# Optimization experiments

Measured on AMD Instinct MI355X. Metric: run time of the kernel, lower is better.

The kernel has to match this reference:

```python
import jax, jax.numpy as jnp
import numpy as np

B, S, T, D, H, DF, E = 16, 1024, 512, 512, 8, 2048, 4
DH = D // H
EPS = 1e-5


def setup_inputs() -> dict:
    key = jax.random.key(0)
    ks = iter(jax.random.split(key, 64))

    def nrm(shape, scale=0.02):
        return jax.random.normal(next(ks), shape, dtype=jnp.float32) * scale

    inp = {
        "x": jax.random.normal(next(ks), (B, S, D), dtype=jnp.float32),
        "cross": jax.random.normal(next(ks), (B, T, D), dtype=jnp.float32),
    }
    for p in ("sa", "ca"):
        for w in ("wq", "wk", "wv", "wo"):
            inp[f"{p}_{w}"] = nrm((D, D))
            inp[f"{p}_b{w[1]}"] = jnp.zeros((D,), jnp.float32)
    inp["gate_w"] = nrm((D, E))
    inp["gate_b"] = jnp.zeros((E,), jnp.float32)
    inp["exp_w1"] = nrm((E, D, DF))
    inp["exp_b1"] = jnp.zeros((E, DF), jnp.float32)
    inp["exp_w2"] = nrm((E, DF, D))
    inp["exp_b2"] = jnp.zeros((E, D), jnp.float32)
    for i in (1, 2, 3):
        inp[f"n{i}_g"] = jnp.ones((D,), jnp.float32)
        inp[f"n{i}_b"] = jnp.zeros((D,), jnp.float32)
    return inp


def layer_norm(x, g, b):
    m = x.mean(-1, keepdims=True)
    v = x.var(-1, keepdims=True)
    return (x - m) * jax.lax.rsqrt(v + EPS) * g + b


def mha(q_in, kv_in, wq, bq, wk, bk, wv, bv, wo, bo, causal):
    Bq, Sq, _ = q_in.shape
    Sk = kv_in.shape[1]
    q = (q_in @ wq + bq).reshape(Bq, Sq, H, DH)
    k = (kv_in @ wk + bk).reshape(Bq, Sk, H, DH)
    v = (kv_in @ wv + bv).reshape(Bq, Sk, H, DH)
    scores = jnp.einsum('bshd,bthd->bhst', q, k) / jnp.sqrt(jnp.float32(DH))
    if causal:
        mask = jnp.tril(jnp.ones((Sq, Sk), dtype=bool))
        scores = jnp.where(mask, scores, jnp.float32(-1e9))
    attn = jax.nn.softmax(scores, axis=-1)
    out = jnp.einsum('bhst,bthd->bshd', attn, v).reshape(Bq, Sq, D)
    return out @ wo + bo


def moe_ffn(x, gw, gb, w1, b1, w2, b2):
    gates = jax.nn.softmax(x @ gw + gb, axis=-1)            # [B,S,E]
    h = jax.nn.relu(jnp.einsum('bsd,edf->bsef', x, w1) + b1)  # [B,S,E,DF]
    yo = jnp.einsum('bsef,efd->bsed', h, w2) + b2            # [B,S,E,D]
    y = jnp.einsum('bse,bsed->bsd', gates, yo)
    imp = gates.mean((0, 1))                                 # importance per expert
    aux = jnp.float32(E) * jnp.sum(imp * imp)                # load-balance penalty
    return y, aux


def reference(x, cross,
              sa_wq, sa_bq, sa_wk, sa_bk, sa_wv, sa_bv, sa_wo, sa_bo,
              ca_wq, ca_bq, ca_wk, ca_bk, ca_wv, ca_bv, ca_wo, ca_bo,
              gate_w, gate_b, exp_w1, exp_b1, exp_w2, exp_b2,
              n1_g, n1_b, n2_g, n2_b, n3_g, n3_b):
    # dropout is identity in eval mode
    x = x + mha(x, x, sa_wq, sa_bq, sa_wk, sa_bk, sa_wv, sa_bv, sa_wo, sa_bo, causal=True)
    x = layer_norm(x, n1_g, n1_b)
    x = x + mha(x, cross, ca_wq, ca_bq, ca_wk, ca_bk, ca_wv, ca_bv, ca_wo, ca_bo, causal=False)
    x = layer_norm(x, n2_g, n2_b)
    y, aux_loss = moe_ffn(x, gate_w, gate_b, exp_w1, exp_b1, exp_w2, exp_b2)
    out = layer_norm(x + y, n3_g, n3_b)
    return out, aux_loss
```

## Files before the change

kernel.cpp:

```cpp
#include <hip/hip_runtime.h>
#include <stdint.h>
#include <stddef.h>

typedef unsigned short bf16u;
typedef __attribute__((ext_vector_type(8))) short short8;
typedef __attribute__((ext_vector_type(4))) float f32x4;

__device__ __forceinline__ bf16u f2bf(float f) {
  union { float f; unsigned u; } v; v.f = f;
  unsigned r = v.u + 0x7FFFu + ((v.u >> 16) & 1u);
  return (bf16u)(r >> 16);
}

#define GL16(g, l) __builtin_amdgcn_global_load_lds( \
    (const __attribute__((address_space(1))) unsigned int*)(g), \
    (__attribute__((address_space(3))) unsigned int*)(l), 16, 0, 0)

enum { EPI_BF16 = 0, EPI_RELU_GATE = 1, EPI_QKV = 2, EPI_RES = 3, EPI_F32ACC = 4, EPI_KV = 5 };

template<int EPI>
__global__ __launch_bounds__(256, 3) void gemm_k(
    const bf16u* __restrict__ A, int LDA,
    const bf16u* __restrict__ BT, int LDB,
    const float* __restrict__ bias, const float* __restrict__ res,
    const float* __restrict__ gates,
    bf16u* __restrict__ o1, bf16u* __restrict__ o2, bf16u* __restrict__ o3,
    float* __restrict__ of,
    int N, int K, int slog, int egate0, int firste)
{
  __shared__ bf16u Ab[2][128 * 32];
  __shared__ bf16u Bb[2][128 * 32];
  const int tid = threadIdx.x, lane = tid & 63, w = tid >> 6;
  const int wm = w >> 1, wn = w & 1;
  const int cpx = gridDim.x >> 3;
  const int bid = (blockIdx.x & 7) * cpx + (blockIdx.x >> 3);
  const int nbt = N >> 7;
  const int mt = bid / nbt, nt = bid - mt * nbt;
  const int bm = mt << 7, bn = nt << 7;

  const int srow = lane >> 2;
  const int scol = (lane & 3) << 3;
  const bf16u* ap0 = A + (size_t)(bm + w * 16 + srow) * LDA + scol;
  const bf16u* ap1 = ap0 + (size_t)64 * LDA;
  const bf16u* bp0 = BT + (size_t)(bn + w * 16 + srow) * LDB + scol;
  const bf16u* bp1 = bp0 + (size_t)64 * LDB;

  f32x4 acc[4][4] = {};
  const int NT = K >> 5;

  GL16(ap0, &Ab[0][w * 512]);
  GL16(ap1, &Ab[0][(4 + w) * 512]);
  GL16(bp0, &Bb[0][w * 512]);
  GL16(bp1, &Bb[0][(4 + w) * 512]);
  __syncthreads();

  const int rl = lane & 15, kg = (lane >> 4) << 3;
  int cur = 0;
  for (int kt = 0; kt < NT; ++kt) {
    if (kt + 1 < NT) {
      const int ko = (kt + 1) << 5;
      const int nb = cur ^ 1;
      GL16(ap0 + ko, &Ab[nb][w * 512]);
      GL16(ap1 + ko, &Ab[nb][(4 + w) * 512]);
      GL16(bp0 + ko, &Bb[nb][w * 512]);
      GL16(bp1 + ko, &Bb[nb][(4 + w) * 512]);
    }
    short8 af[4], bfv[4];
    #pragma unroll
    for (int i = 0; i < 4; ++i)
      af[i] = *(const short8*)&Ab[cur][(wm * 64 + i * 16 + rl) * 32 + kg];
    #pragma unroll
    for (int j = 0; j < 4; ++j)
      bfv[j] = *(const short8*)&Bb[cur][(wn * 64 + j * 16 + rl) * 32 + kg];
    #pragma unroll
    for (int i = 0; i < 4; ++i)
      #pragma unroll
      for (int j = 0; j < 4; ++j)
        acc[i][j] = __builtin_amdgcn_mfma_f32_16x16x32_bf16(af[i], bfv[j], acc[i][j], 0, 0, 0);
    __syncthreads();
    cur ^= 1;
  }

  const int r0 = bm + wm * 64, c0 = bn + wn * 64;
  const int rsub = (lane >> 4) << 2;
  #pragma unroll
  for (int j = 0; j < 4; ++j) {
    const int col = c0 + j * 16 + rl;
    const float bs = bias ? bias[col] : 0.f;
    #pragma unroll
    for (int i = 0; i < 4; ++i) {
      const f32x4 v = acc[i][j];
      #pragma unroll
      for (int jj = 0; jj < 4; ++jj) {
        const int row = r0 + i * 16 + rsub + jj;
        const float val = v[jj] + bs;
        if (EPI == EPI_BF16) {
          o1[(size_t)row * N + col] = f2bf(val);
        } else if (EPI == EPI_RELU_GATE) {
          const float g = gates[(size_t)row * 4 + egate0 + (col >> 11)];
          o1[(size_t)row * N + col] = f2bf(g * (val > 0.f ? val : 0.f));
        } else if (EPI == EPI_QKV) {
          if (col < 512) o1[(size_t)row * 512 + col] = f2bf(val);
          else if (col < 1024) o2[(size_t)row * 512 + col - 512] = f2bf(val);
          else {
            const int c = col - 1024;
            const int b_ = row >> slog, t_ = row & ((1 << slog) - 1);
            o3[(((size_t)(b_ * 8 + (c >> 6)) << 6) + (size_t)(c & 63)) * ((size_t)1 << slog) + t_] = f2bf(val);
          }
        } else if (EPI == EPI_KV) {
          if (col < 512) o2[(size_t)row * 512 + col] = f2bf(val);
          else {
            const int c = col - 512;
            const int b_ = row >> slog, t_ = row & ((1 << slog) - 1);
            o3[(((size_t)(b_ * 8 + (c >> 6)) << 6) + (size_t)(c & 63)) * ((size_t)1 << slog) + t_] = f2bf(val);
          }
        } else if (EPI == EPI_RES) {
          of[(size_t)row * N + col] = res[(size_t)row * N + col] + val;
        } else {
          const size_t oi = (size_t)row * N + col;
          of[oi] = firste ? val : (of[oi] + val);
        }
      }
    }
  }
}

template<bool CAUSAL>
__global__ __launch_bounds__(256, 4) void attn_k(
    const bf16u* __restrict__ Q, const bf16u* __restrict__ Kg,
    const bf16u* __restrict__ VT, bf16u* __restrict__ O,
    int Sq, int Sk)
{
  __shared__ bf16u Kl[2][64 * 64];
  __shared__ bf16u Vl[2][64 * 64];
  __shared__ bf16u Pl[64 * 64];
  const int nqt = Sq >> 6;
  const int cpx = gridDim.x >> 3;
  const int bid = (blockIdx.x & 7) * cpx + (blockIdx.x >> 3);
  const int bh = bid / nqt;
  int qt = bid - bh * nqt;
  if (CAUSAL) qt = nqt - 1 - qt;
  const int b = bh >> 3, h = bh & 7;
  const int tid = threadIdx.x, lane = tid & 63, w = tid >> 6;
  const int rl = lane & 15, g4 = lane >> 4;

  const int qrow = qt * 64 + w * 16 + rl;
  const bf16u* qp = Q + (size_t)(b * Sq + qrow) * 512 + h * 64 + g4 * 8;
  const short8 qf0 = *(const short8*)qp;
  const short8 qf1 = *(const short8*)(qp + 32);

  f32x4 oacc[4] = {};
  float ml = -1e30f, ll = 0.f;
  const int KT = CAUSAL ? (qt + 1) : (Sk >> 6);

  const int str = tid >> 2, stc = tid & 3;
  const int sw_st = (str & 7) << 4;
  const bf16u* kq = Kg + (size_t)(b * Sk + str) * 512 + h * 64 + stc * 8;
  const bf16u* vq = VT + (size_t)(bh * 64 + str) * Sk + stc * 8;
  const int lo0 = str * 128 + ((stc * 16) ^ sw_st);
  const int lo1 = str * 128 + ((stc * 16 + 64) ^ sw_st);

  const int qr = w * 16 + rl;
  char* const pbase = (char*)Pl + qr * 128;
  const int swq = (qr & 7) << 4;

  {
    const short8 k0 = *(const short8*)kq;
    const short8 k1 = *(const short8*)(kq + 32);
    const short8 v0 = *(const short8*)vq;
    const short8 v1 = *(const short8*)(vq + 32);
    *(short8*)((char*)Kl[0] + lo0) = k0;
    *(short8*)((char*)Kl[0] + lo1) = k1;
    *(short8*)((char*)Vl[0] + lo0) = v0;
    *(short8*)((char*)Vl[0] + lo1) = v1;
  }
  __syncthreads();

  int cur = 0;
  for (int kt = 0; kt < KT; ++kt) {
    short8 nk0, nk1, nv0, nv1;
    const bool pre = (kt + 1 < KT);
    if (pre) {
      const bf16u* ks = kq + (size_t)(kt + 1) * 64 * 512;
      const bf16u* vs = vq + (kt + 1) * 64;
      nk0 = *(const short8*)ks;
      nk1 = *(const short8*)(ks + 32);
      nv0 = *(const short8*)vs;
      nv1 = *(const short8*)(vs + 32);
    }

    const bf16u* Kc = Kl[cur];
    const bf16u* Vc = Vl[cur];
    f32x4 st[4] = {};
    #pragma unroll
    for (int mi = 0; mi < 4; ++mi) {
      const int kr = mi * 16 + rl;
      const char* kb_ = (const char*)Kc + kr * 128;
      const int sw = (kr & 7) << 4;
      const short8 kf0 = *(const short8*)(kb_ + ((g4 * 16) ^ sw));
      const short8 kf1 = *(const short8*)(kb_ + ((g4 * 16 + 64) ^ sw));
      st[mi] = __builtin_amdgcn_mfma_f32_16x16x32_bf16(kf0, qf0, st[mi], 0, 0, 0);
      st[mi] = __builtin_amdgcn_mfma_f32_16x16x32_bf16(kf1, qf1, st[mi], 0, 0, 0);
    }

    const float SC = 0.125f * 1.44269504f;
    float sv[16];
    float pm = -1e30f;
    if (CAUSAL && kt == qt) {
      const int qg = qt * 64 + qr;
      #pragma unroll
      for (int mi = 0; mi < 4; ++mi)
        #pragma unroll
        for (int jj = 0; jj < 4; ++jj) {
          float s = st[mi][jj] * SC;
          const int kgi = kt * 64 + mi * 16 + g4 * 4 + jj;
          if (kgi > qg) s = -1e30f;
          sv[mi * 4 + jj] = s;
          pm = fmaxf(pm, s);
        }
    } else {
      #pragma unroll
      for (int mi = 0; mi < 4; ++mi)
        #pragma unroll
        for (int jj = 0; jj < 4; ++jj) {
          const float s = st[mi][jj] * SC;
          sv[mi * 4 + jj] = s;
          pm = fmaxf(pm, s);
        }
    }
    pm = fmaxf(pm, __shfl_xor(pm, 16));
    pm = fmaxf(pm, __shfl_xor(pm, 32));
    const float mnew = fmaxf(ml, pm);
    const float alpha = exp2f(ml - mnew);
    float ps = 0.f;
    bf16u pb[16];
    #pragma unroll
    for (int ii = 0; ii < 16; ++ii) {
      const float p = exp2f(sv[ii] - mnew);
      ps += p;
      pb[ii] = f2bf(p);
    }
    ps += __shfl_xor(ps, 16);
    ps += __shfl_xor(ps, 32);
    ll = ll * alpha + ps;
    ml = mnew;

    #pragma unroll
    for (int jj = 0; jj < 4; ++jj) {
      const float aj = __shfl(alpha, g4 * 4 + jj);
      #pragma unroll
      for (int ni = 0; ni < 4; ++ni) oacc[ni][jj] *= aj;
    }

    #pragma unroll
    for (int mi = 0; mi < 4; ++mi) {
      #pragma unroll
      for (int jp = 0; jp < 2; ++jp) {
        const unsigned pk = (unsigned)pb[mi * 4 + jp * 2] | ((unsigned)pb[mi * 4 + jp * 2 + 1] << 16);
        const int kx2 = mi * 32 + g4 * 8 + jp * 4;
        *(unsigned*)(pbase + (kx2 ^ swq)) = pk;
      }
    }
    asm volatile("s_waitcnt lgkmcnt(0)" ::: "memory");
    #pragma unroll
    for (int ks = 0; ks < 2; ++ks) {
      const short8 pf = *(const short8*)(pbase + ((g4 * 16 + ks * 64) ^ swq));
      #pragma unroll
      for (int ni = 0; ni < 4; ++ni) {
        const int vr = ni * 16 + rl;
        const short8 vf = *(const short8*)((const char*)Vc + vr * 128 + ((g4 * 16 + ks * 64) ^ ((vr & 7) << 4)));
        oacc[ni] = __builtin_amdgcn_mfma_f32_16x16x32_bf16(pf, vf, oacc[ni], 0, 0, 0);
      }
    }

    if (pre) {
      const int nb = cur ^ 1;
      *(short8*)((char*)Kl[nb] + lo0) = nk0;
      *(short8*)((char*)Kl[nb] + lo1) = nk1;
      *(short8*)((char*)Vl[nb] + lo0) = nv0;
      *(short8*)((char*)Vl[nb] + lo1) = nv1;
    }
    __syncthreads();
    cur ^= 1;
  }

  #pragma unroll
  for (int jj = 0; jj < 4; ++jj) {
    const float lj = __shfl(ll, g4 * 4 + jj);
    const float inv = 1.f / lj;
    const int row = qt * 64 + w * 16 + g4 * 4 + jj;
    #pragma unroll
    for (int ni = 0; ni < 4; ++ni)
      O[(size_t)(b * Sq + row) * 512 + h * 64 + ni * 16 + rl] = f2bf(oacc[ni][jj] * inv);
  }
}

template<bool ADD, bool BOUT>
__global__ __launch_bounds__(256, 4) void ln_k(
    const float* __restrict__ X, const float* __restrict__ Y,
    const float* __restrict__ gam, const float* __restrict__ bet,
    float* __restrict__ outf, bf16u* __restrict__ outb)
{
  const int row = blockIdx.x * 4 + (threadIdx.x >> 6);
  const int lane = threadIdx.x & 63;
  const float* xp = X + (size_t)row * 512 + lane * 8;
  float v[8];
  {
    const float4 t0 = *(const float4*)xp;
    const float4 t1 = *(const float4*)(xp + 4);
    v[0] = t0.x; v[1] = t0.y; v[2] = t0.z; v[3] = t0.w;
    v[4] = t1.x; v[5] = t1.y; v[6] = t1.z; v[7] = t1.w;
  }
  if (ADD) {
    const float* yp = Y + (size_t)row * 512 + lane * 8;
    const float4 t0 = *(const float4*)yp;
    const float4 t1 = *(const float4*)(yp + 4);
    v[0] += t0.x; v[1] += t0.y; v[2] += t0.z; v[3] += t0.w;
    v[4] += t1.x; v[5] += t1.y; v[6] += t1.z; v[7] += t1.w;
  }
  float s = 0.f, q = 0.f;
  #pragma unroll
  for (int i = 0; i < 8; ++i) { s += v[i]; q += v[i] * v[i]; }
  #pragma unroll
  for (int off = 1; off < 64; off <<= 1) {
    s += __shfl_xor(s, off);
    q += __shfl_xor(q, off);
  }
  const float mean = s * (1.f / 512.f);
  const float var = q * (1.f / 512.f) - mean * mean;
  const float rs = rsqrtf(var + 1e-5f);
  float o[8];
  #pragma unroll
  for (int i = 0; i < 8; ++i) {
    const float g = gam[lane * 8 + i], bb = bet[lane * 8 + i];
    o[i] = (v[i] - mean) * rs * g + bb;
  }
  float* op = outf + (size_t)row * 512 + lane * 8;
  *(float4*)op = make_float4(o[0], o[1], o[2], o[3]);
  *(float4*)(op + 4) = make_float4(o[4], o[5], o[6], o[7]);
  if (BOUT) {
    union { bf16u u[8]; short8 v8; } pk;
    #pragma unroll
    for (int i = 0; i < 8; ++i) pk.u[i] = f2bf(o[i]);
    *(short8*)(outb + (size_t)row * 512 + lane * 8) = pk.v8;
  }
}

__global__ __launch_bounds__(256, 4) void ln_final_k(
    const float* __restrict__ X, const float* __restrict__ Y,
    const float* __restrict__ gates, const float* __restrict__ b2,
    const float* __restrict__ gam, const float* __restrict__ bet,
    float* __restrict__ outf)
{
  const int row = blockIdx.x * 4 + (threadIdx.x >> 6);
  const int lane = threadIdx.x & 63;
  const float4 gv4 = *(const float4*)(gates + (size_t)row * 4);
  float v[8];
  {
    const float* xp = X + (size_t)row * 512 + lane * 8;
    const float* yp = Y + (size_t)row * 512 + lane * 8;
    const float4 t0 = *(const float4*)xp;
    const float4 t1 = *(const float4*)(xp + 4);
    const float4 u0 = *(const float4*)yp;
    const float4 u1 = *(const float4*)(yp + 4);
    v[0] = t0.x + u0.x; v[1] = t0.y + u0.y; v[2] = t0.z + u0.z; v[3] = t0.w + u0.w;
    v[4] = t1.x + u1.x; v[5] = t1.y + u1.y; v[6] = t1.z + u1.z; v[7] = t1.w + u1.w;
  }
  #pragma unroll
  for (int e = 0; e < 4; ++e) {
    const float ge = e == 0 ? gv4.x : e == 1 ? gv4.y : e == 2 ? gv4.z : gv4.w;
    const float4 b0 = *(const float4*)(b2 + e * 512 + lane * 8);
    const float4 b1 = *(const float4*)(b2 + e * 512 + lane * 8 + 4);
    v[0] += ge * b0.x; v[1] += ge * b0.y; v[2] += ge * b0.z; v[3] += ge * b0.w;
    v[4] += ge * b1.x; v[5] += ge * b1.y; v[6] += ge * b1.z; v[7] += ge * b1.w;
  }
  float s = 0.f, q = 0.f;
  #pragma unroll
  for (int i = 0; i < 8; ++i) { s += v[i]; q += v[i] * v[i]; }
  #pragma unroll
  for (int off = 1; off < 64; off <<= 1) {
    s += __shfl_xor(s, off);
    q += __shfl_xor(q, off);
  }
  const float mean = s * (1.f / 512.f);
  const float var = q * (1.f / 512.f) - mean * mean;
  const float rs = rsqrtf(var + 1e-5f);
  float* op = outf + (size_t)row * 512 + lane * 8;
  float o[8];
  #pragma unroll
  for (int i = 0; i < 8; ++i)
    o[i] = (v[i] - mean) * rs * gam[lane * 8 + i] + bet[lane * 8 + i];
  *(float4*)op = make_float4(o[0], o[1], o[2], o[3]);
  *(float4*)(op + 4) = make_float4(o[4], o[5], o[6], o[7]);
}

__global__ __launch_bounds__(256, 4) void gate_k(
    const float* __restrict__ X, const float* __restrict__ gw,
    const float* __restrict__ gb, float* __restrict__ gates,
    float* __restrict__ imp)
{
  __shared__ float sh[4];
  const int tid = threadIdx.x;
  if (tid < 4) sh[tid] = 0.f;
  __syncthreads();
  const int row = blockIdx.x * 4 + (tid >> 6);
  const int lane = tid & 63;
  const float* xr = X + (size_t)row * 512;
  float a0 = 0.f, a1 = 0.f, a2 = 0.f, a3 = 0.f;
  for (int d = lane; d < 512; d += 64) {
    const float xv = xr[d];
    const float4 wv = *(const float4*)(gw + d * 4);
    a0 += xv * wv.x; a1 += xv * wv.y; a2 += xv * wv.z; a3 += xv * wv.w;
  }
  #pragma unroll
  for (int off = 1; off < 64; off <<= 1) {
    a0 += __shfl_xor(a0, off); a1 += __shfl_xor(a1, off);
    a2 += __shfl_xor(a2, off); a3 += __shfl_xor(a3, off);
  }
  if (lane == 0) {
    a0 += gb[0]; a1 += gb[1]; a2 += gb[2]; a3 += gb[3];
    const float m = fmaxf(fmaxf(a0, a1), fmaxf(a2, a3));
    const float e0 = exp2f((a0 - m) * 1.44269504f);
    const float e1 = exp2f((a1 - m) * 1.44269504f);
    const float e2 = exp2f((a2 - m) * 1.44269504f);
    const float e3 = exp2f((a3 - m) * 1.44269504f);
    const float inv = 1.f / (e0 + e1 + e2 + e3);
    float* gr = gates + (size_t)row * 4;
    const float g0 = e0 * inv, g1 = e1 * inv, g2 = e2 * inv, g3 = e3 * inv;
    gr[0] = g0; gr[1] = g1; gr[2] = g2; gr[3] = g3;
    atomicAdd(&sh[0], g0); atomicAdd(&sh[1], g1);
    atomicAdd(&sh[2], g2); atomicAdd(&sh[3], g3);
  }
  __syncthreads();
  if (tid < 4) atomicAdd(&imp[tid], sh[tid]);
}

__global__ void aux_k(const float* __restrict__ imp, float* __restrict__ out) {
  if (threadIdx.x == 0 && blockIdx.x == 0) {
    float s = 0.f;
    #pragma unroll
    for (int e = 0; e < 4; ++e) { const float v = imp[e] * (1.f / 16384.f); s += v * v; }
    out[0] = 4.f * s;
  }
}

__global__ __launch_bounds__(256, 4) void conv_k(const float* __restrict__ in, bf16u* __restrict__ out) {
  const size_t i = ((size_t)blockIdx.x * 256 + threadIdx.x) * 8;
  const float4 a = *(const float4*)(in + i);
  const float4 b = *(const float4*)(in + i + 4);
  union { bf16u u[8]; short8 v; } pk;
  pk.u[0] = f2bf(a.x); pk.u[1] = f2bf(a.y); pk.u[2] = f2bf(a.z); pk.u[3] = f2bf(a.w);
  pk.u[4] = f2bf(b.x); pk.u[5] = f2bf(b.y); pk.u[6] = f2bf(b.z); pk.u[7] = f2bf(b.w);
  *(short8*)(out + i) = pk.v;
}

__global__ __launch_bounds__(256, 4) void trans_k(
    const float* __restrict__ W, bf16u* __restrict__ WT, int K, int N)
{
  __shared__ float t[32][33];
  const int tx = threadIdx.x & 31, ty = threadIdx.x >> 5;
  const int n0 = blockIdx.x * 32, k0 = blockIdx.y * 32;
  #pragma unroll
  for (int i = 0; i < 4; ++i)
    t[ty + i * 8][tx] = W[(size_t)(k0 + ty + i * 8) * N + n0 + tx];
  __syncthreads();
  #pragma unroll
  for (int i = 0; i < 4; ++i)
    WT[(size_t)(n0 + ty + i * 8) * K + k0 + tx] = f2bf(t[tx][ty + i * 8]);
}

extern "C" void kernel_launch(void* const* d_in, const int* in_sizes, int n_in,
                              void* d_out, int out_size, void* d_ws, size_t ws_size,
                              hipStream_t stream)
{
  const int B = 16, S = 1024, T = 512, D = 512, DF = 2048, E = 4;
  const int M = B * S;
  const int Mc = B * T;
  (void)in_sizes; (void)n_in; (void)out_size;

  const float* x      = (const float*)d_in[0];
  const float* cross  = (const float*)d_in[1];
  const float* gate_w = (const float*)d_in[18];
  const float* gate_b = (const float*)d_in[19];
  const float* exp_w1 = (const float*)d_in[20];
  const float* exp_b1 = (const float*)d_in[21];
  const float* exp_w2 = (const float*)d_in[22];
  const float* exp_b2 = (const float*)d_in[23];

  char* p = (char*)d_ws;
  auto alloc = [&](size_t bytes) -> char* {
    char* r = p;
    p += (bytes + 255) & ~(size_t)255;
    return r;
  };
  bf16u* w1T   = (bf16u*)alloc((size_t)E * DF * D * 2);
  bf16u* w2T   = (bf16u*)alloc((size_t)D * E * DF * 2);
  float* xf    = (float*)alloc((size_t)M * D * 4);
  bf16u* x2b   = (bf16u*)alloc((size_t)M * D * 2);
  float* gates = (float*)alloc((size_t)M * 4 * 4);
  float* imp   = (float*)alloc(256);
  float* y     = (float*)alloc((size_t)M * D * 4);
  float* qkvb  = (float*)alloc(1536 * 4);
  float* kvb   = (float*)alloc(1024 * 4);

  char* upool = p;
  bf16u* xb  = (bf16u*)upool;
  bf16u* crb = xb  + (size_t)M * D;
  bf16u* wT  = crb + (size_t)Mc * D;
  bf16u* qb  = wT  + (size_t)8 * D * D;
  bf16u* kb  = qb  + (size_t)M * D;
  bf16u* vTb = kb  + (size_t)M * D;
  bf16u* ao  = vTb + (size_t)M * D;
  const size_t attnPool = ((size_t)M * D * 5 + (size_t)Mc * D + (size_t)8 * D * D) * 2;
  bf16u* hbuf = (bf16u*)upool;
  const size_t persistent = (size_t)(upool - (char*)d_ws);
  const size_t perE = (size_t)M * DF * 2;
  const size_t rem = ws_size > persistent ? ws_size - persistent : 0;
  const int EC = (rem >= 4 * perE && rem >= attnPool) ? 4
               : (rem >= 2 * perE && rem >= attnPool) ? 2 : 1;

  hipMemsetAsync(imp, 0, 32, stream);
  hipMemcpyAsync(qkvb,        d_in[3], 512 * 4, hipMemcpyDeviceToDevice, stream);
  hipMemcpyAsync(qkvb + 512,  d_in[5], 512 * 4, hipMemcpyDeviceToDevice, stream);
  hipMemcpyAsync(qkvb + 1024, d_in[7], 512 * 4, hipMemcpyDeviceToDevice, stream);
  hipMemcpyAsync(kvb,         d_in[13], 512 * 4, hipMemcpyDeviceToDevice, stream);
  hipMemcpyAsync(kvb + 512,   d_in[15], 512 * 4, hipMemcpyDeviceToDevice, stream);

  conv_k<<<(M * D) / 2048, 256, 0, stream>>>(x, xb);
  conv_k<<<(Mc * D) / 2048, 256, 0, stream>>>(cross, crb);
  for (int i = 0; i < 8; ++i)
    trans_k<<<dim3(D / 32, D / 32), 256, 0, stream>>>((const float*)d_in[2 + 2 * i], wT + (size_t)i * D * D, D, D);
  for (int e = 0; e < E; ++e)
    trans_k<<<dim3(DF / 32, D / 32), 256, 0, stream>>>(exp_w1 + (size_t)e * D * DF, w1T + (size_t)e * DF * D, D, DF);
  trans_k<<<dim3(D / 32, (E * DF) / 32), 256, 0, stream>>>(exp_w2, w2T, E * DF, D);

  const int gATT = B * 8 * (S / 64);

  gemm_k<EPI_QKV><<<(M / 128) * 12, 256, 0, stream>>>(
      xb, 512, wT, 512, qkvb, nullptr, nullptr, qb, kb, vTb, nullptr, 1536, 512, 10, 0, 0);
  attn_k<true><<<gATT, 256, 0, stream>>>(qb, kb, vTb, ao, S, S);
  gemm_k<EPI_RES><<<(M / 128) * 4, 256, 0, stream>>>(
      ao, 512, wT + 3 * (size_t)D * D, 512, (const float*)d_in[9], x, nullptr,
      nullptr, nullptr, nullptr, xf, 512, 512, 0, 0, 0);
  ln_k<false, true><<<M / 4, 256, 0, stream>>>(xf, nullptr, (const float*)d_in[24], (const float*)d_in[25], xf, x2b);

  gemm_k<EPI_BF16><<<(M / 128) * 4, 256, 0, stream>>>(
      x2b, 512, wT + 4 * (size_t)D * D, 512, (const float*)d_in[11], nullptr, nullptr,
      qb, nullptr, nullptr, nullptr, 512, 512, 0, 0, 0);
  gemm_k<EPI_KV><<<(Mc / 128) * 8, 256, 0, stream>>>(
      crb, 512, wT + 5 * (size_t)D * D, 512, kvb, nullptr, nullptr,
      nullptr, kb, vTb, nullptr, 1024, 512, 9, 0, 0);
  attn_k<false><<<gATT, 256, 0, stream>>>(qb, kb, vTb, ao, S, T);
  gemm_k<EPI_RES><<<(M / 128) * 4, 256, 0, stream>>>(
      ao, 512, wT + 7 * (size_t)D * D, 512, (const float*)d_in[17], xf, nullptr,
      nullptr, nullptr, nullptr, xf, 512, 512, 0, 0, 0);
  ln_k<false, true><<<M / 4, 256, 0, stream>>>(xf, nullptr, (const float*)d_in[26], (const float*)d_in[27], xf, x2b);

  gate_k<<<M / 4, 256, 0, stream>>>(xf, gate_w, gate_b, gates, imp);
  aux_k<<<1, 64, 0, stream>>>(imp, (float*)d_out + (size_t)M * D);
  const int NC = E / EC;
  const int Nh = EC * DF;
  for (int c = 0; c < NC; ++c) {
    gemm_k<EPI_RELU_GATE><<<(M / 128) * (Nh / 128), 256, 0, stream>>>(
        x2b, 512, w1T + (size_t)c * Nh * D, 512, exp_b1 + (size_t)c * Nh, nullptr, gates,
        hbuf, nullptr, nullptr, nullptr, Nh, 512, 0, c * EC, 0);
    gemm_k<EPI_F32ACC><<<(M / 128) * 4, 256, 0, stream>>>(
        hbuf, Nh, w2T + (size_t)c * Nh, E * DF, nullptr, nullptr, nullptr,
        nullptr, nullptr, nullptr, y, 512, Nh, 0, 0, c == 0 ? 1 : 0);
  }
  ln_final_k<<<M / 4, 256, 0, stream>>>(xf, y, gates, exp_b2, (const float*)d_in[28], (const float*)d_in[29], (float*)d_out);
}
```

Before: 893.6 us.

## Process 128 query rows per attention block, fuse gating into LayerNorm, batch transposes

The attention kernel now handles two 64-row query tiles per block, so each K/V tile staged in shared memory is reused across 128 queries. In the causal case the first tile skips its fully masked diagonal step. The gating softmax and importance accumulation move into the second LayerNorm kernel, which removes a separate pass over the activations. The weight-transpose launches are batched through a z grid dimension. In exchange the attention kernel carries doubled accumulators and register pressure, lowers launch bounds to 3 blocks per SM, and launches half as many blocks.

Result: slower. 962.9 us (+7.8%).

```diff
diff --git a/kernel.cpp b/kernel.cpp
--- a/kernel.cpp
+++ b/kernel.cpp
@@ -125,16 +125,59 @@
   }
 }
 
+#define SOFTMAX_G(stv, mlv, llv, oaccv, pbX, DOMASK, QG)                      \
+  {                                                                           \
+    float sv[16]; float pm = -1e30f;                                          \
+    _Pragma("unroll")                                                         \
+    for (int mi = 0; mi < 4; ++mi) {                                          \
+      _Pragma("unroll")                                                       \
+      for (int jj = 0; jj < 4; ++jj) {                                        \
+        float s_ = stv[mi][jj] * SC;                                          \
+        if (DOMASK) {                                                         \
+          const int kgi = kt * 64 + mi * 16 + g4 * 4 + jj;                    \
+          if (kgi > (QG)) s_ = -1e30f;                                        \
+        }                                                                     \
+        sv[mi * 4 + jj] = s_; pm = fmaxf(pm, s_);                             \
+      }                                                                       \
+    }                                                                         \
+    pm = fmaxf(pm, __shfl_xor(pm, 16));                                       \
+    pm = fmaxf(pm, __shfl_xor(pm, 32));                                       \
+    const float mnew = fmaxf(mlv, pm);                                        \
+    const float alpha = exp2f(mlv - mnew);                                    \
+    float ps = 0.f;                                                           \
+    _Pragma("unroll")                                                         \
+    for (int mi = 0; mi < 4; ++mi) {                                          \
+      const float p0_ = exp2f(sv[mi * 4 + 0] - mnew);                         \
+      const float p1_ = exp2f(sv[mi * 4 + 1] - mnew);                         \
+      const float p2_ = exp2f(sv[mi * 4 + 2] - mnew);                         \
+      const float p3_ = exp2f(sv[mi * 4 + 3] - mnew);                         \
+      ps += (p0_ + p1_) + (p2_ + p3_);                                        \
+      const unsigned w0_ = (unsigned)f2bf(p0_) | ((unsigned)f2bf(p1_) << 16); \
+      const unsigned w1_ = (unsigned)f2bf(p2_) | ((unsigned)f2bf(p3_) << 16); \
+      *(unsigned*)(pbX + ((mi * 32 + g4 * 8 + 0) ^ swq)) = w0_;               \
+      *(unsigned*)(pbX + ((mi * 32 + g4 * 8 + 4) ^ swq)) = w1_;               \
+    }                                                                         \
+    ps += __shfl_xor(ps, 16);                                                 \
+    ps += __shfl_xor(ps, 32);                                                 \
+    llv = llv * alpha + ps; mlv = mnew;                                       \
+    _Pragma("unroll")                                                         \
+    for (int jj = 0; jj < 4; ++jj) {                                          \
+      const float aj = __shfl(alpha, g4 * 4 + jj);                            \
+      _Pragma("unroll")                                                       \
+      for (int ni = 0; ni < 4; ++ni) oaccv[ni][jj] *= aj;                     \
+    }                                                                         \
+  }
+
 template<bool CAUSAL>
-__global__ __launch_bounds__(256, 4) void attn_k(
+__global__ __launch_bounds__(256, 3) void attn_k(
     const bf16u* __restrict__ Q, const bf16u* __restrict__ Kg,
     const bf16u* __restrict__ VT, bf16u* __restrict__ O,
     int Sq, int Sk)
 {
   __shared__ bf16u Kl[2][64 * 64];
   __shared__ bf16u Vl[2][64 * 64];
-  __shared__ bf16u Pl[64 * 64];
-  const int nqt = Sq >> 6;
+  __shared__ bf16u Pl[128 * 64];
+  const int nqt = Sq >> 7;
   const int cpx = gridDim.x >> 3;
   const int bid = (blockIdx.x & 7) * cpx + (blockIdx.x >> 3);
   const int bh = bid / nqt;
@@ -144,14 +187,19 @@
   const int tid = threadIdx.x, lane = tid & 63, w = tid >> 6;
   const int rl = lane & 15, g4 = lane >> 4;
 
-  const int qrow = qt * 64 + w * 16 + rl;
-  const bf16u* qp = Q + (size_t)(b * Sq + qrow) * 512 + h * 64 + g4 * 8;
-  const short8 qf0 = *(const short8*)qp;
-  const short8 qf1 = *(const short8*)(qp + 32);
-
-  f32x4 oacc[4] = {};
-  float ml = -1e30f, ll = 0.f;
-  const int KT = CAUSAL ? (qt + 1) : (Sk >> 6);
+  const int qr = w * 16 + rl;
+  const int qbase = qt * 128;
+
+  const bf16u* qp0 = Q + (size_t)(b * Sq + qbase + qr) * 512 + h * 64 + g4 * 8;
+  const bf16u* qp1 = qp0 + (size_t)64 * 512;
+  const short8 qa0 = *(const short8*)qp0;
+  const short8 qa1 = *(const short8*)(qp0 + 32);
+  const short8 qc0 = *(const short8*)qp1;
+  const short8 qc1 = *(const short8*)(qp1 + 32);
+
+  f32x4 oacc0[4] = {}, oacc1[4] = {};
+  float ml0 = -1e30f, ll0 = 0.f, ml1 = -1e30f, ll1 = 0.f;
+  const int KT = CAUSAL ? (2 * qt + 2) : (Sk >> 6);
 
   const int str = tid >> 2, stc = tid & 3;
   const int sw_st = (str & 7) << 4;
@@ -160,9 +208,10 @@
   const int lo0 = str * 128 + ((stc * 16) ^ sw_st);
   const int lo1 = str * 128 + ((stc * 16 + 64) ^ sw_st);
 
-  const int qr = w * 16 + rl;
-  char* const pbase = (char*)Pl + qr * 128;
+  char* const pb0 = (char*)Pl + qr * 128;
+  char* const pb1 = (char*)Pl + (64 + qr) * 128;
   const int swq = (qr & 7) << 4;
+  const float SC = 0.125f * 1.44269504f;
 
   {
     const short8 k0 = *(const short8*)kq;
@@ -189,9 +238,13 @@
       nv1 = *(const short8*)(vs + 32);
     }
 
+    const bool mask0 = CAUSAL && (kt == 2 * qt);
+    const bool skip0 = CAUSAL && (kt == 2 * qt + 1);
+    const bool mask1 = CAUSAL && (kt == 2 * qt + 1);
+
     const bf16u* Kc = Kl[cur];
     const bf16u* Vc = Vl[cur];
-    f32x4 st[4] = {};
+    f32x4 st0[4] = {}, st1[4] = {};
     #pragma unroll
     for (int mi = 0; mi < 4; ++mi) {
       const int kr = mi * 16 + rl;
@@ -199,77 +252,28 @@
       const int sw = (kr & 7) << 4;
       const short8 kf0 = *(const short8*)(kb_ + ((g4 * 16) ^ sw));
       const short8 kf1 = *(const short8*)(kb_ + ((g4 * 16 + 64) ^ sw));
-      st[mi] = __builtin_amdgcn_mfma_f32_16x16x32_bf16(kf0, qf0, st[mi], 0, 0, 0);
-      st[mi] = __builtin_amdgcn_mfma_f32_16x16x32_bf16(kf1, qf1, st[mi], 0, 0, 0);
-    }
-
-    const float SC = 0.125f * 1.44269504f;
-    float sv[16];
-    float pm = -1e30f;
-    if (CAUSAL && kt == qt) {
-      const int qg = qt * 64 + qr;
-      #pragma unroll
-      for (int mi = 0; mi < 4; ++mi)
-        #pragma unroll
-        for (int jj = 0; jj < 4; ++jj) {
-          float s = st[mi][jj] * SC;
-          const int kgi = kt * 64 + mi * 16 + g4 * 4 + jj;
-          if (kgi > qg) s = -1e30f;
-          sv[mi * 4 + jj] = s;
-          pm = fmaxf(pm, s);
-        }
-    } else {
-      #pragma unroll
-      for (int mi = 0; mi < 4; ++mi)
-        #pragma unroll
-        for (int jj = 0; jj < 4; ++jj) {
-          const float s = st[mi][jj] * SC;
-          sv[mi * 4 + jj] = s;
-          pm = fmaxf(pm, s);
-        }
-    }
-    pm = fmaxf(pm, __shfl_xor(pm, 16));
-    pm = fmaxf(pm, __shfl_xor(pm, 32));
-    const float mnew = fmaxf(ml, pm);
-    const float alpha = exp2f(ml - mnew);
-    float ps = 0.f;
-    bf16u pb[16];
-    #pragma unroll
-    for (int ii = 0; ii < 16; ++ii) {
-      const float p = exp2f(sv[ii] - mnew);
-      ps += p;
-      pb[ii] = f2bf(p);
-    }
-    ps += __shfl_xor(ps, 16);
-    ps += __shfl_xor(ps, 32);
-    ll = ll * alpha + ps;
-    ml = mnew;
-
-    #pragma unroll
-    for (int jj = 0; jj < 4; ++jj) {
-      const float aj = __shfl(alpha, g4 * 4 + jj);
-      #pragma unroll
-      for (int ni = 0; ni < 4; ++ni) oacc[ni][jj] *= aj;
-    }
-
-    #pragma unroll
-    for (int mi = 0; mi < 4; ++mi) {
-      #pragma unroll
-      for (int jp = 0; jp < 2; ++jp) {
-        const unsigned pk = (unsigned)pb[mi * 4 + jp * 2] | ((unsigned)pb[mi * 4 + jp * 2 + 1] << 16);
-        const int kx2 = mi * 32 + g4 * 8 + jp * 4;
-        *(unsigned*)(pbase + (kx2 ^ swq)) = pk;
+      if (!skip0) {
+        st0[mi] = __builtin_amdgcn_mfma_f32_16x16x32_bf16(kf0, qa0, st0[mi], 0, 0, 0);
+        st0[mi] = __builtin_amdgcn_mfma_f32_16x16x32_bf16(kf1, qa1, st0[mi], 0, 0, 0);
       }
-    }
+      st1[mi] = __builtin_amdgcn_mfma_f32_16x16x32_bf16(kf0, qc0, st1[mi], 0, 0, 0);
+      st1[mi] = __builtin_amdgcn_mfma_f32_16x16x32_bf16(kf1, qc1, st1[mi], 0, 0, 0);
+    }
+
+    if (!skip0) SOFTMAX_G(st0, ml0, ll0, oacc0, pb0, mask0, qbase + qr);
+    SOFTMAX_G(st1, ml1, ll1, oacc1, pb1, mask1, qbase + 64 + qr);
+
     asm volatile("s_waitcnt lgkmcnt(0)" ::: "memory");
     #pragma unroll
     for (int ks = 0; ks < 2; ++ks) {
-      const short8 pf = *(const short8*)(pbase + ((g4 * 16 + ks * 64) ^ swq));
+      const short8 pf0 = *(const short8*)(pb0 + ((g4 * 16 + ks * 64) ^ swq));
+      const short8 pf1 = *(const short8*)(pb1 + ((g4 * 16 + ks * 64) ^ swq));
       #pragma unroll
       for (int ni = 0; ni < 4; ++ni) {
         const int vr = ni * 16 + rl;
         const short8 vf = *(const short8*)((const char*)Vc + vr * 128 + ((g4 * 16 + ks * 64) ^ ((vr & 7) << 4)));
-        oacc[ni] = __builtin_amdgcn_mfma_f32_16x16x32_bf16(pf, vf, oacc[ni], 0, 0, 0);
+        if (!skip0) oacc0[ni] = __builtin_amdgcn_mfma_f32_16x16x32_bf16(pf0, vf, oacc0[ni], 0, 0, 0);
+        oacc1[ni] = __builtin_amdgcn_mfma_f32_16x16x32_bf16(pf1, vf, oacc1[ni], 0, 0, 0);
       }
     }
 
@@ -286,23 +290,34 @@
 
   #pragma unroll
   for (int jj = 0; jj < 4; ++jj) {
-    const float lj = __shfl(ll, g4 * 4 + jj);
-    const float inv = 1.f / lj;
-    const int row = qt * 64 + w * 16 + g4 * 4 + jj;
-    #pragma unroll
-    for (int ni = 0; ni < 4; ++ni)
-      O[(size_t)(b * Sq + row) * 512 + h * 64 + ni * 16 + rl] = f2bf(oacc[ni][jj] * inv);
-  }
-}
-
-template<bool ADD, bool BOUT>
+    const float l0 = __shfl(ll0, g4 * 4 + jj);
+    const float l1 = __shfl(ll1, g4 * 4 + jj);
+    const float i0 = 1.f / l0, i1 = 1.f / l1;
+    const int row = qbase + w * 16 + g4 * 4 + jj;
+    #pragma unroll
+    for (int ni = 0; ni < 4; ++ni) {
+      O[(size_t)(b * Sq + row) * 512 + h * 64 + ni * 16 + rl] = f2bf(oacc0[ni][jj] * i0);
+      O[(size_t)(b * Sq + row + 64) * 512 + h * 64 + ni * 16 + rl] = f2bf(oacc1[ni][jj] * i1);
+    }
+  }
+}
+
+template<bool ADD, bool BOUT, bool GATE>
 __global__ __launch_bounds__(256, 4) void ln_k(
     const float* __restrict__ X, const float* __restrict__ Y,
     const float* __restrict__ gam, const float* __restrict__ bet,
-    float* __restrict__ outf, bf16u* __restrict__ outb)
+    float* __restrict__ outf, bf16u* __restrict__ outb,
+    const float* __restrict__ gw, const float* __restrict__ gb,
+    float* __restrict__ gates, float* __restrict__ imp)
 {
-  const int row = blockIdx.x * 4 + (threadIdx.x >> 6);
-  const int lane = threadIdx.x & 63;
+  __shared__ float sh[4];
+  const int tid = threadIdx.x;
+  if (GATE) {
+    if (tid < 4) sh[tid] = 0.f;
+    __syncthreads();
+  }
+  const int row = blockIdx.x * 4 + (tid >> 6);
+  const int lane = tid & 63;
   const float* xp = X + (size_t)row * 512 + lane * 8;
   float v[8];
   {
@@ -331,10 +346,8 @@
   const float rs = rsqrtf(var + 1e-5f);
   float o[8];
   #pragma unroll
-  for (int i = 0; i < 8; ++i) {
-    const float g = gam[lane * 8 + i], bb = bet[lane * 8 + i];
-    o[i] = (v[i] - mean) * rs * g + bb;
-  }
+  for (int i = 0; i < 8; ++i)
+    o[i] = (v[i] - mean) * rs * gam[lane * 8 + i] + bet[lane * 8 + i];
   float* op = outf + (size_t)row * 512 + lane * 8;
   *(float4*)op = make_float4(o[0], o[1], o[2], o[3]);
   *(float4*)(op + 4) = make_float4(o[4], o[5], o[6], o[7]);
@@ -343,6 +356,35 @@
     #pragma unroll
     for (int i = 0; i < 8; ++i) pk.u[i] = f2bf(o[i]);
     *(short8*)(outb + (size_t)row * 512 + lane * 8) = pk.v8;
+  }
+  if (GATE) {
+    float a0 = 0.f, a1 = 0.f, a2 = 0.f, a3 = 0.f;
+    #pragma unroll
+    for (int i = 0; i < 8; ++i) {
+      const float4 wv = *(const float4*)(gw + (lane * 8 + i) * 4);
+      a0 += o[i] * wv.x; a1 += o[i] * wv.y; a2 += o[i] * wv.z; a3 += o[i] * wv.w;
+    }
+    #pragma unroll
+    for (int off = 1; off < 64; off <<= 1) {
+      a0 += __shfl_xor(a0, off); a1 += __shfl_xor(a1, off);
+      a2 += __shfl_xor(a2, off); a3 += __shfl_xor(a3, off);
+    }
+    if (lane == 0) {
+      a0 += gb[0]; a1 += gb[1]; a2 += gb[2]; a3 += gb[3];
+      const float m = fmaxf(fmaxf(a0, a1), fmaxf(a2, a3));
+      const float e0 = exp2f((a0 - m) * 1.44269504f);
+      const float e1 = exp2f((a1 - m) * 1.44269504f);
+      const float e2 = exp2f((a2 - m) * 1.44269504f);
+      const float e3 = exp2f((a3 - m) * 1.44269504f);
+      const float inv = 1.f / (e0 + e1 + e2 + e3);
+      float* gr = gates + (size_t)row * 4;
+      const float g0 = e0 * inv, g1 = e1 * inv, g2 = e2 * inv, g3 = e3 * inv;
+      gr[0] = g0; gr[1] = g1; gr[2] = g2; gr[3] = g3;
+      atomicAdd(&sh[0], g0); atomicAdd(&sh[1], g1);
+      atomicAdd(&sh[2], g2); atomicAdd(&sh[3], g3);
+    }
+    __syncthreads();
+    if (tid < 4) atomicAdd(&imp[tid], sh[tid]);
   }
 }
 
@@ -394,47 +436,6 @@
   *(float4*)(op + 4) = make_float4(o[4], o[5], o[6], o[7]);
 }
 
-__global__ __launch_bounds__(256, 4) void gate_k(
-    const float* __restrict__ X, const float* __restrict__ gw,
-    const float* __restrict__ gb, float* __restrict__ gates,
-    float* __restrict__ imp)
-{
-  __shared__ float sh[4];
-  const int tid = threadIdx.x;
-  if (tid < 4) sh[tid] = 0.f;
-  __syncthreads();
-  const int row = blockIdx.x * 4 + (tid >> 6);
-  const int lane = tid & 63;
-  const float* xr = X + (size_t)row * 512;
-  float a0 = 0.f, a1 = 0.f, a2 = 0.f, a3 = 0.f;
-  for (int d = lane; d < 512; d += 64) {
-    const float xv = xr[d];
-    const float4 wv = *(const float4*)(gw + d * 4);
-    a0 += xv * wv.x; a1 += xv * wv.y; a2 += xv * wv.z; a3 += xv * wv.w;
-  }
-  #pragma unroll
-  for (int off = 1; off < 64; off <<= 1) {
-    a0 += __shfl_xor(a0, off); a1 += __shfl_xor(a1, off);
-    a2 += __shfl_xor(a2, off); a3 += __shfl_xor(a3, off);
-  }
-  if (lane == 0) {
-    a0 += gb[0]; a1 += gb[1]; a2 += gb[2]; a3 += gb[3];
-    const float m = fmaxf(fmaxf(a0, a1), fmaxf(a2, a3));
-    const float e0 = exp2f((a0 - m) * 1.44269504f);
-    const float e1 = exp2f((a1 - m) * 1.44269504f);
-    const float e2 = exp2f((a2 - m) * 1.44269504f);
-    const float e3 = exp2f((a3 - m) * 1.44269504f);
-    const float inv = 1.f / (e0 + e1 + e2 + e3);
-    float* gr = gates + (size_t)row * 4;
-    const float g0 = e0 * inv, g1 = e1 * inv, g2 = e2 * inv, g3 = e3 * inv;
-    gr[0] = g0; gr[1] = g1; gr[2] = g2; gr[3] = g3;
-    atomicAdd(&sh[0], g0); atomicAdd(&sh[1], g1);
-    atomicAdd(&sh[2], g2); atomicAdd(&sh[3], g3);
-  }
-  __syncthreads();
-  if (tid < 4) atomicAdd(&imp[tid], sh[tid]);
-}
-
 __global__ void aux_k(const float* __restrict__ imp, float* __restrict__ out) {
   if (threadIdx.x == 0 && blockIdx.x == 0) {
     float s = 0.f;
@@ -454,9 +455,31 @@
   *(short8*)(out + i) = pk.v;
 }
 
-__global__ __launch_bounds__(256, 4) void trans_k(
-    const float* __restrict__ W, bf16u* __restrict__ WT, int K, int N)
+struct P8 { const float* w[8]; };
+
+__global__ __launch_bounds__(256, 4) void trans8_k(
+    P8 ps, bf16u* __restrict__ WT0, int K, int N)
 {
+  const float* W = ps.w[blockIdx.z];
+  bf16u* WT = WT0 + (size_t)blockIdx.z * K * N;
+  __shared__ float t[32][33];
+  const int tx = threadIdx.x & 31, ty = threadIdx.x >> 5;
+  const int n0 = blockIdx.x * 32, k0 = blockIdx.y * 32;
+  #pragma unroll
+  for (int i = 0; i < 4; ++i)
+    t[ty + i * 8][tx] = W[(size_t)(k0 + ty + i * 8) * N + n0 + tx];
+  __syncthreads();
+  #pragma unroll
+  for (int i = 0; i < 4; ++i)
+    WT[(size_t)(n0 + ty + i * 8) * K + k0 + tx] = f2bf(t[tx][ty + i * 8]);
+}
+
+__global__ __launch_bounds__(256, 4) void trans_s_k(
+    const float* __restrict__ W0, size_t wstride,
+    bf16u* __restrict__ WT0, size_t tstride, int K, int N)
+{
+  const float* W = W0 + (size_t)blockIdx.z * wstride;
+  bf16u* WT = WT0 + (size_t)blockIdx.z * tstride;
   __shared__ float t[32][33];
   const int tx = threadIdx.x & 31, ty = threadIdx.x >> 5;
   const int n0 = blockIdx.x * 32, k0 = blockIdx.y * 32;
@@ -528,13 +551,17 @@
 
   conv_k<<<(M * D) / 2048, 256, 0, stream>>>(x, xb);
   conv_k<<<(Mc * D) / 2048, 256, 0, stream>>>(cross, crb);
-  for (int i = 0; i < 8; ++i)
-    trans_k<<<dim3(D / 32, D / 32), 256, 0, stream>>>((const float*)d_in[2 + 2 * i], wT + (size_t)i * D * D, D, D);
-  for (int e = 0; e < E; ++e)
-    trans_k<<<dim3(DF / 32, D / 32), 256, 0, stream>>>(exp_w1 + (size_t)e * D * DF, w1T + (size_t)e * DF * D, D, DF);
-  trans_k<<<dim3(D / 32, (E * DF) / 32), 256, 0, stream>>>(exp_w2, w2T, E * DF, D);
-
-  const int gATT = B * 8 * (S / 64);
+  {
+    P8 ps;
+    for (int i = 0; i < 8; ++i) ps.w[i] = (const float*)d_in[2 + 2 * i];
+    trans8_k<<<dim3(D / 32, D / 32, 8), 256, 0, stream>>>(ps, wT, D, D);
+  }
+  trans_s_k<<<dim3(DF / 32, D / 32, 4), 256, 0, stream>>>(
+      exp_w1, (size_t)D * DF, w1T, (size_t)DF * D, D, DF);
+  trans_s_k<<<dim3(D / 32, (E * DF) / 32, 1), 256, 0, stream>>>(
+      exp_w2, 0, w2T, 0, E * DF, D);
+
+  const int gATT = B * 8 * (S / 128);
 
   gemm_k<EPI_QKV><<<(M / 128) * 12, 256, 0, stream>>>(
       xb, 512, wT, 512, qkvb, nullptr, nullptr, qb, kb, vTb, nullptr, 1536, 512, 10, 0, 0);
@@ -542,7 +569,9 @@
   gemm_k<EPI_RES><<<(M / 128) * 4, 256, 0, stream>>>(
       ao, 512, wT + 3 * (size_t)D * D, 512, (const float*)d_in[9], x, nullptr,
       nullptr, nullptr, nullptr, xf, 512, 512, 0, 0, 0);
-  ln_k<false, true><<<M / 4, 256, 0, stream>>>(xf, nullptr, (const float*)d_in[24], (const float*)d_in[25], xf, x2b);
+  ln_k<false, true, false><<<M / 4, 256, 0, stream>>>(
+      xf, nullptr, (const float*)d_in[24], (const float*)d_in[25], xf, x2b,
+      nullptr, nullptr, nullptr, nullptr);
 
   gemm_k<EPI_BF16><<<(M / 128) * 4, 256, 0, stream>>>(
       x2b, 512, wT + 4 * (size_t)D * D, 512, (const float*)d_in[11], nullptr, nullptr,
@@ -554,9 +583,10 @@
   gemm_k<EPI_RES><<<(M / 128) * 4, 256, 0, stream>>>(
       ao, 512, wT + 7 * (size_t)D * D, 512, (const float*)d_in[17], xf, nullptr,
       nullptr, nullptr, nullptr, xf, 512, 512, 0, 0, 0);
-  ln_k<false, true><<<M / 4, 256, 0, stream>>>(xf, nullptr, (const float*)d_in[26], (const float*)d_in[27], xf, x2b);
-
-  gate_k<<<M / 4, 256, 0, stream>>>(xf, gate_w, gate_b, gates, imp);
+  ln_k<false, true, true><<<M / 4, 256, 0, stream>>>(
+      xf, nullptr, (const float*)d_in[26], (const float*)d_in[27], xf, x2b,
+      gate_w, gate_b, gates, imp);
+
   aux_k<<<1, 64, 0, stream>>>(imp, (float*)d_out + (size_t)M * D);
   const int NC = E / EC;
   const int Nh = EC * DF;
```
